# Kernel optimization log

Measured on AMD Instinct MI355X. Metric: run time of the kernel, lower is better.

Reference implementation:

```python
import jax, jax.numpy as jnp
import numpy as np

B, T, D_IN = 32, 512, 150
D, L, H = 512, 8, 8
HD = D // H
FF = 4 * D
LLM = 512
TXT = 20


def _layernorm(x, g, b, eps=1e-5):
    m = jnp.mean(x, -1, keepdims=True)
    v = jnp.var(x, -1, keepdims=True)
    return (x - m) * jax.lax.rsqrt(v + eps) * g + b


def _timestep_pe(t, d):
    # sinusoidal PE of the diffusion step, interleaved sin/cos (torch PositionalEncoding)
    pos = t.astype(jnp.float32)[:, None]
    div = jnp.exp(-jnp.log(10000.0) * jnp.arange(0, d, 2, dtype=jnp.float32) / d)
    ang = pos * div
    return jnp.stack([jnp.sin(ang), jnp.cos(ang)], -1).reshape(t.shape[0], d)


def _rope_cos_sin(t, hd):
    inv = 1.0 / (10000.0 ** (jnp.arange(0, hd, 2, dtype=jnp.float32) / hd))
    ang = jnp.arange(t, dtype=jnp.float32)[:, None] * inv  # [T, hd/2]
    ang = jnp.concatenate([ang, ang], -1)  # [T, hd]
    return jnp.cos(ang), jnp.sin(ang)


def _apply_rope(x, cos, sin):
    # x: [B,H,T,hd]; rotate-half convention
    x1, x2 = jnp.split(x, 2, -1)
    rot = jnp.concatenate([-x2, x1], -1)
    return x * cos + rot * sin


def setup_inputs() -> dict:
    key = jax.random.key(0)
    ks = iter(jax.random.split(key, 64))
    nrm = lambda shape: jax.random.normal(next(ks), shape, jnp.float32) * 0.02
    return {
        "x": jax.random.normal(next(ks), (B, T, D_IN), jnp.float32),
        "timesteps": jax.random.randint(next(ks), (B,), 0, 1000),
        "enc_text": jax.random.normal(next(ks), (B, TXT, LLM), jnp.float32),
        "W_in": nrm((D_IN, D)), "b_in": jnp.zeros((D,), jnp.float32),
        "W_t1": nrm((D, D)), "b_t1": jnp.zeros((D,), jnp.float32),
        "W_t2": nrm((D, D)), "b_t2": jnp.zeros((D,), jnp.float32),
        "W_txt": nrm((LLM, D)), "b_txt": jnp.zeros((D,), jnp.float32),
        "ln1_g": jnp.ones((L, D), jnp.float32), "ln1_b": jnp.zeros((L, D), jnp.float32),
        "Wqkv": nrm((L, D, 3 * D)), "bqkv": jnp.zeros((L, 3 * D), jnp.float32),
        "Wo": nrm((L, D, D)), "bo": jnp.zeros((L, D), jnp.float32),
        "ln2_g": jnp.ones((L, D), jnp.float32), "ln2_b": jnp.zeros((L, D), jnp.float32),
        "W1": nrm((L, D, FF)), "b1": jnp.zeros((L, FF), jnp.float32),
        "W2": nrm((L, FF, D)), "b2": jnp.zeros((L, D), jnp.float32),
        "W_out": nrm((D, D_IN)), "b_out": jnp.zeros((D_IN,), jnp.float32),
    }


def reference(x, timesteps, enc_text, W_in, b_in, W_t1, b_t1, W_t2, b_t2,
              W_txt, b_txt, ln1_g, ln1_b, Wqkv, bqkv, Wo, bo,
              ln2_g, ln2_b, W1, b1, W2, b2, W_out, b_out):
    # conditioning fusion: timestep PE -> SiLU MLP, text mean-pool -> linear, summed
    t_emb = _timestep_pe(timesteps, D)
    t_emb = jax.nn.silu(t_emb @ W_t1 + b_t1) @ W_t2 + b_t2  # [B,D]
    txt_emb = jnp.mean(enc_text, axis=1) @ W_txt + b_txt      # [B,D]
    emb = t_emb + txt_emb
    # input process + broadcast conditioning over frames (RoPE carries positions)
    h = x @ W_in + b_in + emb[:, None, :]  # [B,T,D]
    cos, sin = _rope_cos_sin(T, HD)
    scale = 1.0 / jnp.sqrt(jnp.float32(HD))
    for i in range(L):  # 8 structurally identical pre-LN RoPE encoder blocks
        y = _layernorm(h, ln1_g[i], ln1_b[i])
        q, k, v = jnp.split(y @ Wqkv[i] + bqkv[i], 3, -1)
        q = q.reshape(B, T, H, HD).transpose(0, 2, 1, 3)
        k = k.reshape(B, T, H, HD).transpose(0, 2, 1, 3)
        v = v.reshape(B, T, H, HD).transpose(0, 2, 1, 3)
        q = _apply_rope(q, cos, sin)
        k = _apply_rope(k, cos, sin)
        attn = jax.nn.softmax(jnp.einsum('bhqd,bhkd->bhqk', q, k) * scale, -1)
        o = jnp.einsum('bhqk,bhkd->bhqd', attn, v).transpose(0, 2, 1, 3).reshape(B, T, D)
        h = h + o @ Wo[i] + bo[i]
        y = _layernorm(h, ln2_g[i], ln2_b[i])
        h = h + jax.nn.gelu(y @ W1[i] + b1[i], approximate=False) @ W2[i] + b2[i]
    return h @ W_out + b_out  # [B,T,input_feats]
```

## Files before the change

kernel.cpp:

```cpp
#include <hip/hip_runtime.h>
#include <hip/hip_bf16.h>
#include <math.h>

typedef unsigned short u16;
typedef __attribute__((ext_vector_type(8))) short bf16x8;
typedef __attribute__((ext_vector_type(4))) float f32x4;

__device__ __forceinline__ u16 f2b(float x) {
  union { float f; unsigned u; } c; c.f = x;
  unsigned r = c.u + 0x7FFFu + ((c.u >> 16) & 1u);
  return (u16)(r >> 16);
}
__device__ __forceinline__ float b2f(u16 u) {
  union { unsigned u; float f; } c; c.u = ((unsigned)u) << 16;
  return c.f;
}

__device__ __forceinline__ void gl_lds16(const u16* g, u16* l) {
  __builtin_amdgcn_global_load_lds(
      (const __attribute__((address_space(1))) void*)g,
      (__attribute__((address_space(3))) void*)l, 16, 0, 0);
}

__global__ void tconv(const float* __restrict__ W, u16* __restrict__ WT,
                      int K, int N, int KApad, int Npad) {
  __shared__ float tile[32][33];
  int z = blockIdx.z;
  W += (size_t)z * K * N;
  WT += (size_t)z * Npad * KApad;
  int n0 = blockIdx.x * 32, k0 = blockIdx.y * 32;
  int tx = threadIdx.x, ty = threadIdx.y;
  for (int i = 0; i < 4; ++i) {
    int k = k0 + ty + i * 8, n = n0 + tx;
    tile[ty + i * 8][tx] = (k < K && n < N) ? W[(size_t)k * N + n] : 0.f;
  }
  __syncthreads();
  for (int i = 0; i < 4; ++i) {
    int n = n0 + ty + i * 8, k = k0 + tx;
    WT[(size_t)n * KApad + k] = f2b(tile[tx][ty + i * 8]);
  }
}

__global__ void cond1(const int* __restrict__ ts, const float* __restrict__ Wt1,
                      const float* __restrict__ bt1, float* __restrict__ t1) {
  __shared__ float pe[512];
  int b = blockIdx.x, tid = threadIdx.x;
  float pos = (float)ts[b];
  int i2 = tid >> 1;
  float dv = expf(-0.0359778920780e0f * (float)i2);
  float ang = pos * dv;
  pe[tid] = (tid & 1) ? cosf(ang) : sinf(ang);
  __syncthreads();
  float acc = bt1[tid];
  for (int k = 0; k < 512; ++k) acc += pe[k] * Wt1[k * 512 + tid];
  t1[b * 512 + tid] = acc / (1.f + expf(-acc));
}

__global__ void cond2(const float* __restrict__ t1buf, const float* __restrict__ Wt2,
                      const float* __restrict__ bt2, const float* __restrict__ enc,
                      const float* __restrict__ Wtxt, const float* __restrict__ btxt,
                      float* __restrict__ emb) {
  __shared__ float a[512], m[512];
  int b = blockIdx.x, tid = threadIdx.x;
  a[tid] = t1buf[b * 512 + tid];
  float s = 0.f;
  for (int j = 0; j < 20; ++j) s += enc[((size_t)(b * 20 + j)) * 512 + tid];
  m[tid] = s * 0.05f;
  __syncthreads();
  float acc = bt2[tid] + btxt[tid];
  for (int k = 0; k < 512; ++k) acc += a[k] * Wt2[k * 512 + tid] + m[k] * Wtxt[k * 512 + tid];
  emb[b * 512 + tid] = acc;
}

__global__ void rope_tab(float2* __restrict__ rt) {
  int idx = blockIdx.x * 256 + threadIdx.x;
  int t = idx >> 5, i = idx & 31;
  float ang = (float)t * __expf(-0.28782313662f * (float)i);
  float sn, cn;
  sincosf(ang, &sn, &cn);
  rt[idx] = make_float2(cn, sn);
}

__global__ void xconv(const float* __restrict__ x, u16* __restrict__ xb) {
  int idx = blockIdx.x * 256 + threadIdx.x;
  int mrow = idx / 192, kk = idx - mrow * 192;
  float v = (kk < 150) ? x[(size_t)mrow * 150 + kk] : 0.f;
  xb[idx] = f2b(v);
}

__global__ __launch_bounds__(256) void ln_kernel(const float* __restrict__ h,
                                                 const float* __restrict__ g,
                                                 const float* __restrict__ be,
                                                 u16* __restrict__ y) {
  int w = threadIdx.x >> 6, lane = threadIdx.x & 63;
  int row = blockIdx.x * 4 + w;
  const float* hr = h + (size_t)row * 512 + lane * 8;
  float4 a = ((const float4*)hr)[0], b4 = ((const float4*)hr)[1];
  float s = a.x + a.y + a.z + a.w + b4.x + b4.y + b4.z + b4.w;
  float s2 = a.x * a.x + a.y * a.y + a.z * a.z + a.w * a.w +
             b4.x * b4.x + b4.y * b4.y + b4.z * b4.z + b4.w * b4.w;
#pragma unroll
  for (int o = 32; o; o >>= 1) {
    s += __shfl_xor(s, o, 64);
    s2 += __shfl_xor(s2, o, 64);
  }
  float mean = s * (1.f / 512.f);
  float var = s2 * (1.f / 512.f) - mean * mean;
  float rs = rsqrtf(var + 1e-5f);
  const float4* gp = (const float4*)(g + lane * 8);
  const float4* bp = (const float4*)(be + lane * 8);
  float4 g0 = gp[0], g1 = gp[1], be0 = bp[0], be1 = bp[1];
  ushort4 o0, o1;
  o0.x = f2b((a.x - mean) * rs * g0.x + be0.x);
  o0.y = f2b((a.y - mean) * rs * g0.y + be0.y);
  o0.z = f2b((a.z - mean) * rs * g0.z + be0.z);
  o0.w = f2b((a.w - mean) * rs * g0.w + be0.w);
  o1.x = f2b((b4.x - mean) * rs * g1.x + be1.x);
  o1.y = f2b((b4.y - mean) * rs * g1.y + be1.y);
  o1.z = f2b((b4.z - mean) * rs * g1.z + be1.z);
  o1.w = f2b((b4.w - mean) * rs * g1.w + be1.w);
  ushort4* yp = (ushort4*)(y + (size_t)row * 512 + lane * 8);
  yp[0] = o0;
  yp[1] = o1;
}

__global__ __launch_bounds__(256) void attn_mfma2(const u16* __restrict__ qk,
                                                  const u16* __restrict__ vt,
                                                  u16* __restrict__ o) {
  __shared__ u16 Qs[64 * 64];
  __shared__ u16 KVs[128 * 64];
  __shared__ u16 Ps[64 * 128];
  const int tid = threadIdx.x;
  int bid = blockIdx.x;
  const int rr = bid & 7, gg = bid >> 3;
  const int qt = gg & 7;
  const int hb = rr + 8 * (gg >> 3);
  const int h = hb & 7, b = hb >> 3;
  const int lane = tid & 63, w = tid >> 6;
  const int q = lane >> 4, c16 = lane & 15;

  const size_t qbase = (size_t)(b * 512 + qt * 64) * 1024 + h * 64;
  {
    int row0 = tid >> 3, cs = tid & 7;
#pragma unroll
    for (int rep = 0; rep < 2; ++rep) {
      int r2 = rep * 32 + row0;
      int g = cs ^ (r2 & 7);
      gl_lds16(qk + qbase + (size_t)r2 * 1024 + g * 8, Qs + rep * 2048 + tid * 8);
    }
  }

  f32x4 o_acc[4];
  float l_st[4];
#pragma unroll
  for (int jd = 0; jd < 4; ++jd) o_acc[jd] = (f32x4){0.f, 0.f, 0.f, 0.f};
#pragma unroll
  for (int r = 0; r < 4; ++r) l_st[r] = 0.f;

  const size_t kbase = (size_t)b * 512 * 1024 + 512 + h * 64;
  const size_t vtbase = ((size_t)(b * 8 + h) * 64) * 512;

  for (int kt = 0; kt < 4; ++kt) {
    if (kt) __syncthreads();
    {
      int row0 = tid >> 3, cs = tid & 7;
#pragma unroll
      for (int rep = 0; rep < 4; ++rep) {
        int r2 = rep * 32 + row0;
        int g = cs ^ (r2 & 7);
        gl_lds16(qk + kbase + (size_t)(kt * 128 + r2) * 1024 + g * 8,
                 KVs + rep * 2048 + tid * 8);
      }
    }
    __syncthreads();

    f32x4 s_acc[8];
#pragma unroll
    for (int j = 0; j < 8; ++j) s_acc[j] = (f32x4){0.f, 0.f, 0.f, 0.f};
#pragma unroll
    for (int ka = 0; ka < 2; ++ka) {
      bf16x8 af, bf[8];
      {
        int row = w * 16 + c16;
        af = *(const bf16x8*)(Qs + row * 64 + (((ka * 4 + q) ^ (row & 7)) * 8));
      }
#pragma unroll
      for (int j = 0; j < 8; ++j) {
        int row = j * 16 + c16;
        bf[j] = *(const bf16x8*)(KVs + row * 64 + (((ka * 4 + q) ^ (row & 7)) * 8));
      }
#pragma unroll
      for (int j = 0; j < 8; ++j)
        s_acc[j] = __builtin_amdgcn_mfma_f32_16x16x32_bf16(af, bf[j], s_acc[j], 0, 0, 0);
    }
    __syncthreads();

    {
      int vr0 = tid >> 4, cc = tid & 15;
#pragma unroll
      for (int rep = 0; rep < 4; ++rep) {
        int row = rep * 16 + vr0;
        int g2 = cc ^ (row & 15);
        gl_lds16(vt + vtbase + (size_t)row * 512 + kt * 128 + g2 * 8,
                 KVs + rep * 2048 + tid * 8);
      }
    }

#pragma unroll
    for (int r = 0; r < 4; ++r) {
      float sum = 0.f;
#pragma unroll
      for (int j = 0; j < 8; ++j) {
        float p = __expf(s_acc[j][r]);
        s_acc[j][r] = p;
        sum += p;
      }
      l_st[r] += sum;
    }

#pragma unroll
    for (int j = 0; j < 8; ++j)
#pragma unroll
      for (int r = 0; r < 4; ++r) {
        int prow = w * 16 + q * 4 + r;
        int col = j * 16 + c16;
        int cp = col >> 3;
        Ps[prow * 128 + ((cp ^ (prow & 15)) * 8) + (col & 7)] = f2b(s_acc[j][r]);
      }
    __syncthreads();

#pragma unroll
    for (int s = 0; s < 4; ++s) {
      bf16x8 af, bv[4];
      {
        int row = w * 16 + c16;
        af = *(const bf16x8*)(Ps + row * 128 + (((s * 4 + q) ^ (row & 15)) * 8));
      }
#pragma unroll
      for (int jd = 0; jd < 4; ++jd) {
        int row = jd * 16 + c16;
        bv[jd] = *(const bf16x8*)(KVs + row * 128 + (((s * 4 + q) ^ (row & 15)) * 8));
      }
#pragma unroll
      for (int jd = 0; jd < 4; ++jd)
        o_acc[jd] = __builtin_amdgcn_mfma_f32_16x16x32_bf16(af, bv[jd], o_acc[jd], 0, 0, 0);
    }
  }

#pragma unroll
  for (int r = 0; r < 4; ++r) {
    float l = l_st[r];
    l += __shfl_xor(l, 1, 64);
    l += __shfl_xor(l, 2, 64);
    l += __shfl_xor(l, 4, 64);
    l += __shfl_xor(l, 8, 64);
    float inv = 1.f / l;
    int trow = qt * 64 + w * 16 + q * 4 + r;
#pragma unroll
    for (int jd = 0; jd < 4; ++jd)
      o[(size_t)(b * 512 + trow) * 512 + h * 64 + jd * 16 + c16] = f2b(o_acc[jd][r] * inv);
  }
}

template <int MODE, int BM = 128, int BN = 128>
__global__ __launch_bounds__(256) void gemm_bf16(
    const u16* __restrict__ A, const u16* __restrict__ BT,
    const float* __restrict__ bias, const float* aux, void* aux2, void* Cout,
    int KA, int ldc, int nx) {
  __shared__ u16 As[BM * 64];
  __shared__ u16 Bs[BN * 64];
  constexpr int AI = BM / 32;
  constexpr int BJ = BN / 32;
  const int tid = threadIdx.x;
  int bid = blockIdx.x;
  int rr = bid & 7, gg = bid >> 3;
  int xN = gg % nx, yM = rr + 8 * (gg / nx);
  const int tileN = xN * BN;
  const int tileM = yM * BM;
  const int lane = tid & 63, w = tid >> 6;
  const int mw = (w >> 1) * (BM / 2), nw = (w & 1) * (BN / 2);
  const int q = lane >> 4, c16 = lane & 15;

  f32x4 acc[AI][BJ];
#pragma unroll
  for (int i = 0; i < AI; ++i)
#pragma unroll
    for (int j = 0; j < BJ; ++j) acc[i][j] = (f32x4){0.f, 0.f, 0.f, 0.f};

  const int rowA0 = tid >> 3;
  const int cs = tid & 7;
  const int KT = KA >> 6;
  for (int kt = 0; kt < KT; ++kt) {
    __syncthreads();
#pragma unroll
    for (int rep = 0; rep < BM / 32; ++rep) {
      int row = rep * 32 + rowA0;
      int g = cs ^ (row & 7);
      gl_lds16(A + (size_t)(tileM + row) * KA + kt * 64 + g * 8,
               (u16*)((char*)As + rep * 4096 + tid * 16));
    }
#pragma unroll
    for (int rep = 0; rep < BN / 32; ++rep) {
      int row = rep * 32 + rowA0;
      int g = cs ^ (row & 7);
      gl_lds16(BT + (size_t)(tileN + row) * KA + kt * 64 + g * 8,
               (u16*)((char*)Bs + rep * 4096 + tid * 16));
    }
    __syncthreads();
#pragma unroll
    for (int ks = 0; ks < 2; ++ks) {
      bf16x8 af[AI], bfr[BJ];
#pragma unroll
      for (int i = 0; i < AI; ++i) {
        int m = mw + i * 16 + c16;
        int ca = (ks * 4 + q) ^ (m & 7);
        af[i] = *(const bf16x8*)((const char*)As + m * 128 + ca * 16);
      }
#pragma unroll
      for (int j = 0; j < BJ; ++j) {
        int n = nw + j * 16 + c16;
        int cb = (ks * 4 + q) ^ (n & 7);
        bfr[j] = *(const bf16x8*)((const char*)Bs + n * 128 + cb * 16);
      }
#pragma unroll
      for (int i = 0; i < AI; ++i)
#pragma unroll
        for (int j = 0; j < BJ; ++j)
          acc[i][j] = __builtin_amdgcn_mfma_f32_16x16x32_bf16(af[i], bfr[j], acc[i][j], 0, 0, 0);
    }
  }

  if constexpr (MODE == 5) {
    const float2* rt = (const float2*)aux;
    u16* qk = (u16*)Cout;
    u16* vtp = (u16*)aux2;
#pragma unroll
    for (int i = 0; i < AI; ++i) {
      int row = tileM + mw + i * 16 + q * 4;
      int bb = row >> 9, t0 = row & 511;
#pragma unroll
      for (int jp = 0; jp < 2; ++jp) {
        int colA = tileN + nw + jp * 16 + c16;
        if (colA < 1024) {
          int colB = colA + 32;
          int d31 = colA & 31;
          float scl = (colA < 512) ? 0.125f : 1.f;
          float bA = bias[colA], bB = bias[colB];
#pragma unroll
          for (int r = 0; r < 4; ++r) {
            float2 cs2 = rt[(t0 + r) * 32 + d31];
            float x1 = acc[i][jp][r] + bA;
            float x2 = acc[i][jp + 2][r] + bB;
            size_t rbase = (size_t)(row + r) * 1024;
            qk[rbase + colA] = f2b((x1 * cs2.x - x2 * cs2.y) * scl);
            qk[rbase + colB] = f2b((x2 * cs2.x + x1 * cs2.y) * scl);
          }
        } else {
#pragma unroll
          for (int jj = jp; jj < 4; jj += 2) {
            int col = tileN + nw + jj * 16 + c16;
            int hh = (col - 1024) >> 6, d = col & 63;
            float bv2 = bias[col];
            ushort4 pk;
            pk.x = f2b(acc[i][jj][0] + bv2);
            pk.y = f2b(acc[i][jj][1] + bv2);
            pk.z = f2b(acc[i][jj][2] + bv2);
            pk.w = f2b(acc[i][jj][3] + bv2);
            *(ushort4*)(vtp + ((size_t)((bb * 8 + hh) * 64 + d)) * 512 + t0) = pk;
          }
        }
      }
    }
    return;
  }

#pragma unroll
  for (int i = 0; i < AI; ++i) {
#pragma unroll
    for (int j = 0; j < BJ; ++j) {
      int col = tileN + nw + j * 16 + c16;
      float bv = (MODE == 4) ? 0.f : bias[col];
#pragma unroll
      for (int r = 0; r < 4; ++r) {
        int row = tileM + mw + i * 16 + q * 4 + r;
        float v = acc[i][j][r] + bv;
        if (MODE == 0) {
          ((float*)Cout)[(size_t)row * ldc + col] = v + aux[(row >> 9) * 512 + col];
        } else if (MODE == 2) {
          size_t idx = (size_t)row * ldc + col;
          ((float*)Cout)[idx] = aux[idx] + v;
        } else if (MODE == 3) {
          float u = v * v;
          float p = __builtin_fmaf(0.044715f, u, 1.0f);
          float t2 = v * p;
          float e = __expf(-1.59576912f * t2);
          float r2 = __builtin_amdgcn_rcpf(1.0f + e);
          ((u16*)Cout)[(size_t)row * ldc + col] = f2b(v * r2);
        } else if (MODE == 4) {
          if (col < 150) ((float*)Cout)[(size_t)row * 150 + col] = acc[i][j][r] + bias[col];
        } else if (MODE == 6) {
          size_t idx = (size_t)row * ldc + col;
          float v2 = aux[idx] + v;
          ((float*)Cout)[idx] = v2;
          ((u16*)aux2)[idx] = f2b(v2);
        }
      }
    }
  }
}

extern "C" void kernel_launch(void* const* d_in, const int* in_sizes, int n_in,
                              void* d_out, int out_size, void* d_ws, size_t ws_size,
                              hipStream_t stream) {
  const float* x = (const float*)d_in[0];
  const int* tsteps = (const int*)d_in[1];
  const float* enc = (const float*)d_in[2];
  const float* W_in = (const float*)d_in[3];
  const float* b_in = (const float*)d_in[4];
  const float* W_t1 = (const float*)d_in[5];
  const float* b_t1 = (const float*)d_in[6];
  const float* W_t2 = (const float*)d_in[7];
  const float* b_t2 = (const float*)d_in[8];
  const float* W_txt = (const float*)d_in[9];
  const float* b_txt = (const float*)d_in[10];
  const float* ln1_g = (const float*)d_in[11];
  const float* ln1_b = (const float*)d_in[12];
  const float* Wqkv = (const float*)d_in[13];
  const float* bqkv = (const float*)d_in[14];
  const float* Wo = (const float*)d_in[15];
  const float* bo = (const float*)d_in[16];
  const float* ln2_g = (const float*)d_in[17];
  const float* ln2_b = (const float*)d_in[18];
  const float* W1 = (const float*)d_in[19];
  const float* b1 = (const float*)d_in[20];
  const float* W2 = (const float*)d_in[21];
  const float* b2 = (const float*)d_in[22];
  const float* W_out = (const float*)d_in[23];
  const float* b_out = (const float*)d_in[24];

  char* ws = (char*)d_ws;
  u16* WT_in = (u16*)(ws + 0);
  u16* WT_qkv = (u16*)(ws + 196608);
  u16* WT_o = (u16*)(ws + 12779520);
  u16* WT_1 = (u16*)(ws + 16973824);
  u16* WT_2 = (u16*)(ws + 33751040);
  u16* WT_out = (u16*)(ws + 50528256);
  u16* xb = (u16*)(ws + 50790400);
  float* hf = (float*)(ws + 57081856);
  u16* yb = (u16*)(ws + 90636288);
  u16* qkvb = (u16*)(ws + 107413504);
  float2* rtab = (float2*)(ws + 107413504 + 33554432);
  u16* ob = (u16*)(ws + 157745152);
  u16* ffb = (u16*)(ws + 174522368);
  u16* hb = (u16*)(ws + 241631232);
  u16* vtb = hb;
  float* embf = (float*)(ws + 258408448);
  float* t1c = (float*)(ws + 258473984);

  dim3 tb(32, 8);
  tconv<<<dim3(16, 6, 1), tb, 0, stream>>>(W_in, WT_in, 150, 512, 192, 512);
  tconv<<<dim3(48, 16, 8), tb, 0, stream>>>(Wqkv, WT_qkv, 512, 1536, 512, 1536);
  tconv<<<dim3(16, 16, 8), tb, 0, stream>>>(Wo, WT_o, 512, 512, 512, 512);
  tconv<<<dim3(64, 16, 8), tb, 0, stream>>>(W1, WT_1, 512, 2048, 512, 2048);
  tconv<<<dim3(16, 64, 8), tb, 0, stream>>>(W2, WT_2, 2048, 512, 2048, 512);
  tconv<<<dim3(8, 16, 1), tb, 0, stream>>>(W_out, WT_out, 512, 150, 512, 256);

  cond1<<<32, 512, 0, stream>>>(tsteps, W_t1, b_t1, t1c);
  cond2<<<32, 512, 0, stream>>>(t1c, W_t2, b_t2, enc, W_txt, b_txt, embf);
  rope_tab<<<64, 256, 0, stream>>>(rtab);
  xconv<<<12288, 256, 0, stream>>>(x, xb);

  gemm_bf16<0, 64, 128><<<4 * 256, 256, 0, stream>>>(xb, WT_in, b_in, embf, nullptr, hf, 192, 512, 4);

  for (int l = 0; l < 8; ++l) {
    ln_kernel<<<4096, 256, 0, stream>>>(hf, ln1_g + l * 512, ln1_b + l * 512, yb);
    gemm_bf16<5, 128, 128><<<12 * 128, 256, 0, stream>>>(yb, WT_qkv + (size_t)l * 1536 * 512,
                                                         bqkv + l * 1536, (const float*)rtab,
                                                         vtb, qkvb, 512, 1024, 12);
    attn_mfma2<<<2048, 256, 0, stream>>>(qkvb, vtb, ob);
    gemm_bf16<2, 64, 128><<<4 * 256, 256, 0, stream>>>(ob, WT_o + (size_t)l * 512 * 512,
                                                       bo + l * 512, hf, nullptr, hf, 512, 512, 4);
    ln_kernel<<<4096, 256, 0, stream>>>(hf, ln2_g + l * 512, ln2_b + l * 512, yb);
    gemm_bf16<3, 128, 128><<<16 * 128, 256, 0, stream>>>(yb, WT_1 + (size_t)l * 2048 * 512,
                                                         b1 + l * 2048, nullptr, nullptr, ffb,
                                                         512, 2048, 16);
    if (l < 7) {
      gemm_bf16<2, 64, 128><<<4 * 256, 256, 0, stream>>>(ffb, WT_2 + (size_t)l * 512 * 2048,
                                                         b2 + l * 512, hf, nullptr, hf, 2048, 512, 4);
    } else {
      gemm_bf16<6, 64, 128><<<4 * 256, 256, 0, stream>>>(ffb, WT_2 + (size_t)l * 512 * 2048,
                                                         b2 + l * 512, hf, hb, hf, 2048, 512, 4);
    }
  }

  gemm_bf16<4, 64, 128><<<2 * 256, 256, 0, stream>>>(hb, WT_out, b_out, nullptr, nullptr, d_out, 512, 150, 2);
}
```

Before: 2.104 ms.

## Keep Q in registers and read V directly from global in attention

Measured after the change: 2.473 ms. 17.6% more time.

```diff
diff --git a/kernel.cpp b/kernel.cpp
--- a/kernel.cpp
+++ b/kernel.cpp
@@ -127,8 +127,7 @@
 __global__ __launch_bounds__(256) void attn_mfma2(const u16* __restrict__ qk,
                                                   const u16* __restrict__ vt,
                                                   u16* __restrict__ o) {
-  __shared__ u16 Qs[64 * 64];
-  __shared__ u16 KVs[128 * 64];
+  __shared__ u16 Ks[128 * 64];
   __shared__ u16 Ps[64 * 128];
   const int tid = threadIdx.x;
   int bid = blockIdx.x;
@@ -140,14 +139,12 @@
   const int q = lane >> 4, c16 = lane & 15;
 
   const size_t qbase = (size_t)(b * 512 + qt * 64) * 1024 + h * 64;
+  bf16x8 q_reg[2];
   {
-    int row0 = tid >> 3, cs = tid & 7;
-#pragma unroll
-    for (int rep = 0; rep < 2; ++rep) {
-      int r2 = rep * 32 + row0;
-      int g = cs ^ (r2 & 7);
-      gl_lds16(qk + qbase + (size_t)r2 * 1024 + g * 8, Qs + rep * 2048 + tid * 8);
-    }
+    int row = w * 16 + c16;
+#pragma unroll
+    for (int ka = 0; ka < 2; ++ka)
+      q_reg[ka] = *(const bf16x8*)(qk + qbase + (size_t)row * 1024 + (ka * 4 + q) * 8);
   }
 
   f32x4 o_acc[4];
@@ -169,7 +166,7 @@
         int r2 = rep * 32 + row0;
         int g = cs ^ (r2 & 7);
         gl_lds16(qk + kbase + (size_t)(kt * 128 + r2) * 1024 + g * 8,
-                 KVs + rep * 2048 + tid * 8);
+                 Ks + rep * 2048 + tid * 8);
       }
     }
     __syncthreads();
@@ -179,31 +176,15 @@
     for (int j = 0; j < 8; ++j) s_acc[j] = (f32x4){0.f, 0.f, 0.f, 0.f};
 #pragma unroll
     for (int ka = 0; ka < 2; ++ka) {
-      bf16x8 af, bf[8];
-      {
-        int row = w * 16 + c16;
-        af = *(const bf16x8*)(Qs + row * 64 + (((ka * 4 + q) ^ (row & 7)) * 8));
-      }
+      bf16x8 bf[8];
 #pragma unroll
       for (int j = 0; j < 8; ++j) {
         int row = j * 16 + c16;
-        bf[j] = *(const bf16x8*)(KVs + row * 64 + (((ka * 4 + q) ^ (row & 7)) * 8));
+        bf[j] = *(const bf16x8*)(Ks + row * 64 + (((ka * 4 + q) ^ (row & 7)) * 8));
       }
 #pragma unroll
       for (int j = 0; j < 8; ++j)
-        s_acc[j] = __builtin_amdgcn_mfma_f32_16x16x32_bf16(af, bf[j], s_acc[j], 0, 0, 0);
-    }
-    __syncthreads();
-
-    {
-      int vr0 = tid >> 4, cc = tid & 15;
-#pragma unroll
-      for (int rep = 0; rep < 4; ++rep) {
-        int row = rep * 16 + vr0;
-        int g2 = cc ^ (row & 15);
-        gl_lds16(vt + vtbase + (size_t)row * 512 + kt * 128 + g2 * 8,
-                 KVs + rep * 2048 + tid * 8);
-      }
+        s_acc[j] = __builtin_amdgcn_mfma_f32_16x16x32_bf16(q_reg[ka], bf[j], s_acc[j], 0, 0, 0);
     }
 
 #pragma unroll
@@ -227,7 +208,6 @@
         int cp = col >> 3;
         Ps[prow * 128 + ((cp ^ (prow & 15)) * 8) + (col & 7)] = f2b(s_acc[j][r]);
       }
-    __syncthreads();
 
 #pragma unroll
     for (int s = 0; s < 4; ++s) {
@@ -239,7 +219,7 @@
 #pragma unroll
       for (int jd = 0; jd < 4; ++jd) {
         int row = jd * 16 + c16;
-        bv[jd] = *(const bf16x8*)(KVs + row * 128 + (((s * 4 + q) ^ (row & 15)) * 8));
+        bv[jd] = *(const bf16x8*)(vt + vtbase + (size_t)row * 512 + kt * 128 + (s * 4 + q) * 8);
       }
 #pragma unroll
       for (int jd = 0; jd < 4; ++jd)
```
